# Kernel optimization log

Hardware: AMD Instinct MI355X
Metric: run time of the kernel (lower is better)

## Reference

```python
import jax, jax.numpy as jnp
import numpy as np

DIM = 2048
DIM_SEQ = 2048
DIM_OUT = DIM // 2
LN_EPS = 1e-5


def setup_inputs() -> dict:
    key = jax.random.key(0)
    k1, k2 = jax.random.split(key)
    x = jax.random.normal(k1, (8, DIM_SEQ, DIM), dtype=jnp.float32)
    init_eps = 0.001 / DIM_SEQ
    # Conv1d(dim_seq, dim_seq, 1) weight -> [seq, seq] seq-mixing matrix
    proj_w = jax.random.uniform(k2, (DIM_SEQ, DIM_SEQ), minval=-init_eps, maxval=init_eps, dtype=jnp.float32)
    proj_b = jnp.ones((DIM_SEQ,), dtype=jnp.float32)
    ln_scale = jnp.ones((DIM_OUT,), dtype=jnp.float32)
    ln_bias = jnp.zeros((DIM_OUT,), dtype=jnp.float32)
    return {"x": x, "proj_w": proj_w, "proj_b": proj_b, "ln_scale": ln_scale, "ln_bias": ln_bias}


def reference(x, proj_w, proj_b, ln_scale, ln_bias):
    # chunk into residual and gate halves along feature dim
    res, gate = jnp.split(x, 2, axis=-1)  # each [b, s, d/2]
    # LayerNorm over last dim of gate
    mu = jnp.mean(gate, axis=-1, keepdims=True)
    var = jnp.mean(jnp.square(gate - mu), axis=-1, keepdims=True)
    gate = (gate - mu) * jax.lax.rsqrt(var + LN_EPS) * ln_scale + ln_bias
    # Conv1d kernel=1 over seq axis == seq-mixing matmul: [s,t] x [b,t,d] -> [b,s,d]
    gate = jnp.einsum('st,btd->bsd', proj_w, gate) + proj_b[None, :, None]
    # act = Identity; gated residual multiply
    return gate * res
```

## Files before the change

### kernel.cpp

```cpp
#include <hip/hip_runtime.h>

typedef __attribute__((ext_vector_type(4))) float floatx4;
typedef __attribute__((ext_vector_type(2))) unsigned long ulongx2;

__device__ __forceinline__ unsigned short f2bf(float f) {
    unsigned int u = __builtin_bit_cast(unsigned int, f);
    u += 0x7fffu + ((u >> 16) & 1u);
    return (unsigned short)(u >> 16);
}

__device__ __forceinline__ float bf2f(unsigned short u) {
    return __builtin_bit_cast(float, ((unsigned int)u) << 16);
}

__device__ __forceinline__ void async16(void* lds, const void* g) {
    __builtin_amdgcn_global_load_lds(
        (const __attribute__((address_space(1))) void*)(g),
        (__attribute__((address_space(3))) void*)(lds),
        16, 0, 0);
}

#define DIM      2048
#define DSEQ     2048
#define DOUT     1024
#define NBATCH   8
#define NKT      (DSEQ / 64)
#define WSCALE   4194304.0f
#define WINV     (1.0f / 4194304.0f)


__global__ __launch_bounds__(256) void cast_w_kernel(const float* __restrict__ w,
                                                     unsigned char* __restrict__ o) {
    int i = (blockIdx.x * 256 + threadIdx.x) * 4;
    int s = i >> 11;
    int t = i & 2047;
    float4 v = *(const float4*)(w + i);
    int w0 = __builtin_amdgcn_cvt_pk_fp8_f32(v.x * WSCALE, v.y * WSCALE, 0, false);
    w0     = __builtin_amdgcn_cvt_pk_fp8_f32(v.z * WSCALE, v.w * WSCALE, w0, true);
    unsigned char* dst = o + (((size_t)(t >> 6)) * DSEQ + s) * 64
                           + ((t >> 3) & 3) * 16 + ((t >> 5) & 1) * 8 + (t & 7);
    *(unsigned int*)dst = (unsigned int)w0;
}

__global__ __launch_bounds__(256) void ln_t_kernel(const float* __restrict__ X,
                                                   const float* __restrict__ lns,
                                                   const float* __restrict__ lnb,
                                                   unsigned char* __restrict__ Gt) {
    const int tid  = threadIdx.x;
    const int wave = tid >> 6;
    const int lane = tid & 63;
    const int t0   = blockIdx.x * 32;
    const int b    = blockIdx.y;
    const int kt   = t0 >> 6;
    const int h    = (t0 >> 5) & 1;

    __shared__ unsigned short lt[32][1028];

    float4 sc[4], bi[4];
    #pragma unroll
    for (int c = 0; c < 4; ++c) {
        sc[c] = *(const float4*)(lns + c * 256 + lane * 4);
        bi[c] = *(const float4*)(lnb + c * 256 + lane * 4);
    }

    #pragma unroll 1
    for (int i = 0; i < 8; ++i) {
        const int r = wave * 8 + i;
        const float* xr = X + ((size_t)(b * DSEQ + t0 + r)) * DIM + DOUT;
        float4 v[4];
        float s = 0.f, ss = 0.f;
        #pragma unroll
        for (int c = 0; c < 4; ++c) {
            v[c] = *(const float4*)(xr + c * 256 + lane * 4);
            s  += v[c].x + v[c].y + v[c].z + v[c].w;
            ss += v[c].x * v[c].x + v[c].y * v[c].y + v[c].z * v[c].z + v[c].w * v[c].w;
        }
        #pragma unroll
        for (int off = 32; off > 0; off >>= 1) {
            s  += __shfl_xor(s,  off, 64);
            ss += __shfl_xor(ss, off, 64);
        }
        const float mu  = s * (1.f / 1024.f);
        const float var = ss * (1.f / 1024.f) - mu * mu;
        const float inv = rsqrtf(var + 1e-5f);
        #pragma unroll
        for (int c = 0; c < 4; ++c) {
            const int d = c * 256 + lane * 4;
            float y0 = (v[c].x - mu) * inv * sc[c].x + bi[c].x;
            float y1 = (v[c].y - mu) * inv * sc[c].y + bi[c].y;
            float y2 = (v[c].z - mu) * inv * sc[c].z + bi[c].z;
            float y3 = (v[c].w - mu) * inv * sc[c].w + bi[c].w;
            unsigned int lo = (unsigned int)f2bf(y0) | ((unsigned int)f2bf(y1) << 16);
            unsigned int hi = (unsigned int)f2bf(y2) | ((unsigned int)f2bf(y3) << 16);
            *(uint2*)&lt[r][d] = make_uint2(lo, hi);
        }
    }
    __syncthreads();

    #pragma unroll
    for (int it = 0; it < 4; ++it) {
        const int d = it * 256 + tid;
        unsigned char* dst = Gt + (((size_t)b * NKT + kt) * DOUT + d) * 64 + h * 8;
        #pragma unroll
        for (int qq = 0; qq < 4; ++qq) {
            const int lr = qq * 8;
            int w0 = __builtin_amdgcn_cvt_pk_fp8_f32(bf2f(lt[lr + 0][d]), bf2f(lt[lr + 1][d]), 0, false);
            w0     = __builtin_amdgcn_cvt_pk_fp8_f32(bf2f(lt[lr + 2][d]), bf2f(lt[lr + 3][d]), w0, true);
            int w1 = __builtin_amdgcn_cvt_pk_fp8_f32(bf2f(lt[lr + 4][d]), bf2f(lt[lr + 5][d]), 0, false);
            w1     = __builtin_amdgcn_cvt_pk_fp8_f32(bf2f(lt[lr + 6][d]), bf2f(lt[lr + 7][d]), w1, true);
            *(uint2*)(dst + qq * 16) = make_uint2((unsigned int)w0, (unsigned int)w1);
        }
    }
}

#define BM 128
#define BN 128

__global__ __launch_bounds__(256, 3) void gemm_sgu(const unsigned char* __restrict__ Wt,
                                                   const unsigned char* __restrict__ Gt,
                                                   const float* __restrict__ X,
                                                   const float* __restrict__ Pb,
                                                   float* __restrict__ Out) {
    const int tid = threadIdx.x;
    const int ys  = blockIdx.x & 7;
    const int xs  = (blockIdx.x >> 3) | (blockIdx.y << 1);
    const int s0  = xs * BM;
    const int d0  = ys * BN;
    const int b   = blockIdx.z;

    __shared__ __align__(16) unsigned char smem[32768];

    const int wave = tid >> 6;
    const int lane = tid & 63;
    const int wr   = wave >> 1;
    const int wc   = wave & 1;
    const int ln15 = lane & 15;
    const int q    = lane >> 4;

    int ldsOff[2], srcA[2], srcB[2];
    #pragma unroll
    for (int j = 0; j < 2; ++j) {
        const int c  = tid + j * 256;
        const int r  = c >> 2;
        const int kc = (c & 3) ^ (r & 3);
        ldsOff[j] = c * 16;
        srcA[j]   = (s0 + r) * 64 + kc * 16;
        srcB[j]   = (d0 + r) * 64 + kc * 16;
    }
    int aOff[4], bOff[4];
    #pragma unroll
    for (int i = 0; i < 4; ++i) {
        const int ra = wr * 64 + i * 16 + ln15;
        const int rb = wc * 64 + i * 16 + ln15;
        aOff[i] = ra * 64 + ((q ^ (ra & 3)) * 16);
        bOff[i] = rb * 64 + ((q ^ (rb & 3)) * 16);
    }

    floatx4 acc[4][4] = {};

    const unsigned char* gB = Gt + (size_t)b * (NKT * DOUT * 64);

    {
        unsigned char* As = smem;
        unsigned char* Bs = smem + 8192;
        #pragma unroll
        for (int j = 0; j < 2; ++j) {
            async16(As + ldsOff[j], Wt + srcA[j]);
            async16(Bs + ldsOff[j], gB + srcB[j]);
        }
    }

    for (int t = 0; t < NKT; ++t) {
        unsigned char* Ab = smem + (t & 1) * 16384;
        unsigned char* Bb = Ab + 8192;
        __syncthreads();

        if (t + 1 < NKT) {
            const unsigned char* aB0 = Wt + (size_t)(t + 1) * (DSEQ * 64);
            const unsigned char* bB0 = gB + (size_t)(t + 1) * (DOUT * 64);
            unsigned char* An = smem + ((t + 1) & 1) * 16384;
            unsigned char* Bn = An + 8192;
            #pragma unroll
            for (int j = 0; j < 2; ++j) {
                async16(An + ldsOff[j], aB0 + srcA[j]);
                async16(Bn + ldsOff[j], bB0 + srcB[j]);
            }
        }

        ulongx2 a2[4], b2[4];
        #pragma unroll
        for (int i = 0; i < 4; ++i) a2[i] = *(const ulongx2*)(Ab + aOff[i]);
        #pragma unroll
        for (int i = 0; i < 4; ++i) b2[i] = *(const ulongx2*)(Bb + bOff[i]);
        #pragma unroll
        for (int i = 0; i < 4; ++i)
            #pragma unroll
            for (int j = 0; j < 4; ++j)
                acc[i][j] = __builtin_amdgcn_mfma_f32_16x16x32_fp8_fp8(
                    (long)a2[i].x, (long)b2[j].x, acc[i][j], 0, 0, 0);
        #pragma unroll
        for (int i = 0; i < 4; ++i)
            #pragma unroll
            for (int j = 0; j < 4; ++j)
                acc[i][j] = __builtin_amdgcn_mfma_f32_16x16x32_fp8_fp8(
                    (long)a2[i].y, (long)b2[j].y, acc[i][j], 0, 0, 0);
    }

    float (*ep)[132] = (float (*)[132])smem;
    const int gr  = tid >> 3;
    const int seg = tid & 7;
    #pragma unroll
    for (int e = 0; e < 4; ++e) {
        __syncthreads();
        #pragma unroll
        for (int j = 0; j < 4; ++j) {
            const int C = wc * 64 + j * 16 + ln15;
            #pragma unroll
            for (int r = 0; r < 4; ++r)
                ep[wr * 16 + q * 4 + r][C] = acc[e][j][r];
        }
        __syncthreads();
        const int s = s0 + (gr >> 4) * 64 + e * 16 + (gr & 15);
        const int d = d0 + seg * 16;
        const float pb = Pb[s];
        const float* xr = X + ((size_t)(b * DSEQ + s)) * DIM + d;
        float*       orow = Out + ((size_t)(b * DSEQ + s)) * DOUT + d;
        #pragma unroll
        for (int w = 0; w < 4; ++w) {
            float4 c = *(const float4*)&ep[gr][seg * 16 + w * 4];
            float4 x = *(const float4*)(xr + w * 4);
            float4 o;
            o.x = (c.x * WINV + pb) * x.x;
            o.y = (c.y * WINV + pb) * x.y;
            o.z = (c.z * WINV + pb) * x.z;
            o.w = (c.w * WINV + pb) * x.w;
            *(float4*)(orow + w * 4) = o;
        }
    }
}

extern "C" void kernel_launch(void* const* d_in, const int* in_sizes, int n_in,
                              void* d_out, int out_size, void* d_ws, size_t ws_size,
                              hipStream_t stream) {
    const float* x    = (const float*)d_in[0];
    const float* pw   = (const float*)d_in[1];
    const float* pb   = (const float*)d_in[2];
    const float* lns  = (const float*)d_in[3];
    const float* lnb  = (const float*)d_in[4];
    float* out        = (float*)d_out;

    unsigned char* Wt = (unsigned char*)d_ws;
    unsigned char* Gt = (unsigned char*)d_ws + (size_t)DSEQ * DSEQ;

    cast_w_kernel<<<dim3((DSEQ * DSEQ) / 1024), dim3(256), 0, stream>>>(pw, Wt);
    ln_t_kernel<<<dim3(DSEQ / 32, NBATCH), dim3(256), 0, stream>>>(x, lns, lnb, Gt);
    gemm_sgu<<<dim3(16, 8, NBATCH), dim3(256), 0, stream>>>(Wt, Gt, x, pb, out);
}
```

Measured before the change: 271.9 us.

## Switch GEMM to gfx950 scaled 16x16x128 FP8 MFMA with K=128 tiles

```diff
diff --git a/kernel.cpp b/kernel.cpp
--- a/kernel.cpp
+++ b/kernel.cpp
@@ -1,7 +1,8 @@
 #include <hip/hip_runtime.h>
 
 typedef __attribute__((ext_vector_type(4))) float floatx4;
-typedef __attribute__((ext_vector_type(2))) unsigned long ulongx2;
+typedef __attribute__((ext_vector_type(4))) int   intx4;
+typedef __attribute__((ext_vector_type(8))) int   intx8;
 
 __device__ __forceinline__ unsigned short f2bf(float f) {
     unsigned int u = __builtin_bit_cast(unsigned int, f);
@@ -24,9 +25,10 @@
 #define DSEQ     2048
 #define DOUT     1024
 #define NBATCH   8
-#define NKT      (DSEQ / 64)
+#define NKT      (DSEQ / 128)
 #define WSCALE   4194304.0f
 #define WINV     (1.0f / 4194304.0f)
+#define UNIT_SCALE 0x7F7F7F7F
 
 
 __global__ __launch_bounds__(256) void cast_w_kernel(const float* __restrict__ w,
@@ -37,8 +39,7 @@
     float4 v = *(const float4*)(w + i);
     int w0 = __builtin_amdgcn_cvt_pk_fp8_f32(v.x * WSCALE, v.y * WSCALE, 0, false);
     w0     = __builtin_amdgcn_cvt_pk_fp8_f32(v.z * WSCALE, v.w * WSCALE, w0, true);
-    unsigned char* dst = o + (((size_t)(t >> 6)) * DSEQ + s) * 64
-                           + ((t >> 3) & 3) * 16 + ((t >> 5) & 1) * 8 + (t & 7);
+    unsigned char* dst = o + (((size_t)(t >> 7)) * DSEQ + s) * 128 + (t & 127);
     *(unsigned int*)dst = (unsigned int)w0;
 }
 
@@ -51,8 +52,8 @@
     const int lane = tid & 63;
     const int t0   = blockIdx.x * 32;
     const int b    = blockIdx.y;
-    const int kt   = t0 >> 6;
-    const int h    = (t0 >> 5) & 1;
+    const int kt   = t0 >> 7;
+    const int h2   = (t0 >> 5) & 3;
 
     __shared__ unsigned short lt[32][1028];
 
@@ -100,23 +101,24 @@
     #pragma unroll
     for (int it = 0; it < 4; ++it) {
         const int d = it * 256 + tid;
-        unsigned char* dst = Gt + (((size_t)b * NKT + kt) * DOUT + d) * 64 + h * 8;
-        #pragma unroll
-        for (int qq = 0; qq < 4; ++qq) {
-            const int lr = qq * 8;
+        unsigned int u[8];
+        #pragma unroll
+        for (int g = 0; g < 8; ++g) {
+            const int lr = g * 4;
             int w0 = __builtin_amdgcn_cvt_pk_fp8_f32(bf2f(lt[lr + 0][d]), bf2f(lt[lr + 1][d]), 0, false);
             w0     = __builtin_amdgcn_cvt_pk_fp8_f32(bf2f(lt[lr + 2][d]), bf2f(lt[lr + 3][d]), w0, true);
-            int w1 = __builtin_amdgcn_cvt_pk_fp8_f32(bf2f(lt[lr + 4][d]), bf2f(lt[lr + 5][d]), 0, false);
-            w1     = __builtin_amdgcn_cvt_pk_fp8_f32(bf2f(lt[lr + 6][d]), bf2f(lt[lr + 7][d]), w1, true);
-            *(uint2*)(dst + qq * 16) = make_uint2((unsigned int)w0, (unsigned int)w1);
-        }
+            u[g] = (unsigned int)w0;
+        }
+        unsigned char* dst = Gt + (((size_t)b * NKT + kt) * DOUT + d) * 128 + h2 * 32;
+        *(uint4*)(dst)      = make_uint4(u[0], u[1], u[2], u[3]);
+        *(uint4*)(dst + 16) = make_uint4(u[4], u[5], u[6], u[7]);
     }
 }
 
 #define BM 128
 #define BN 128
 
-__global__ __launch_bounds__(256, 3) void gemm_sgu(const unsigned char* __restrict__ Wt,
+__global__ __launch_bounds__(256, 2) void gemm_sgu(const unsigned char* __restrict__ Wt,
                                                    const unsigned char* __restrict__ Gt,
                                                    const float* __restrict__ X,
                                                    const float* __restrict__ Pb,
@@ -128,7 +130,7 @@
     const int d0  = ys * BN;
     const int b   = blockIdx.z;
 
-    __shared__ __align__(16) unsigned char smem[32768];
+    __shared__ __align__(16) unsigned char smem[65536];
 
     const int wave = tid >> 6;
     const int lane = tid & 63;
@@ -137,73 +139,79 @@
     const int ln15 = lane & 15;
     const int q    = lane >> 4;
 
-    int ldsOff[2], srcA[2], srcB[2];
-    #pragma unroll
-    for (int j = 0; j < 2; ++j) {
+    int ldsOff[4], srcA[4], srcB[4];
+    #pragma unroll
+    for (int j = 0; j < 4; ++j) {
         const int c  = tid + j * 256;
-        const int r  = c >> 2;
-        const int kc = (c & 3) ^ (r & 3);
+        const int r  = c >> 3;
+        const int kc = (c & 7) ^ (r & 7);
         ldsOff[j] = c * 16;
-        srcA[j]   = (s0 + r) * 64 + kc * 16;
-        srcB[j]   = (d0 + r) * 64 + kc * 16;
-    }
-    int aOff[4], bOff[4];
+        srcA[j]   = (s0 + r) * 128 + kc * 16;
+        srcB[j]   = (d0 + r) * 128 + kc * 16;
+    }
+    int aOff0[4], aOff1[4], bOff0[4], bOff1[4];
     #pragma unroll
     for (int i = 0; i < 4; ++i) {
         const int ra = wr * 64 + i * 16 + ln15;
         const int rb = wc * 64 + i * 16 + ln15;
-        aOff[i] = ra * 64 + ((q ^ (ra & 3)) * 16);
-        bOff[i] = rb * 64 + ((q ^ (rb & 3)) * 16);
+        aOff0[i] = ra * 128 + ((2 * q)     ^ (ra & 7)) * 16;
+        aOff1[i] = ra * 128 + ((2 * q + 1) ^ (ra & 7)) * 16;
+        bOff0[i] = rb * 128 + ((2 * q)     ^ (rb & 7)) * 16;
+        bOff1[i] = rb * 128 + ((2 * q + 1) ^ (rb & 7)) * 16;
     }
 
     floatx4 acc[4][4] = {};
 
-    const unsigned char* gB = Gt + (size_t)b * (NKT * DOUT * 64);
+    const unsigned char* gB = Gt + (size_t)b * ((size_t)NKT * DOUT * 128);
 
     {
         unsigned char* As = smem;
-        unsigned char* Bs = smem + 8192;
-        #pragma unroll
-        for (int j = 0; j < 2; ++j) {
+        unsigned char* Bs = smem + 16384;
+        #pragma unroll
+        for (int j = 0; j < 4; ++j) {
             async16(As + ldsOff[j], Wt + srcA[j]);
             async16(Bs + ldsOff[j], gB + srcB[j]);
         }
     }
 
     for (int t = 0; t < NKT; ++t) {
-        unsigned char* Ab = smem + (t & 1) * 16384;
-        unsigned char* Bb = Ab + 8192;
+        unsigned char* Ab = smem + (t & 1) * 32768;
+        unsigned char* Bb = Ab + 16384;
         __syncthreads();
 
         if (t + 1 < NKT) {
-            const unsigned char* aB0 = Wt + (size_t)(t + 1) * (DSEQ * 64);
-            const unsigned char* bB0 = gB + (size_t)(t + 1) * (DOUT * 64);
-            unsigned char* An = smem + ((t + 1) & 1) * 16384;
-            unsigned char* Bn = An + 8192;
+            const unsigned char* aB0 = Wt + (size_t)(t + 1) * (DSEQ * 128);
+            const unsigned char* bB0 = gB + (size_t)(t + 1) * (DOUT * 128);
+            unsigned char* An = smem + ((t + 1) & 1) * 32768;
+            unsigned char* Bn = An + 16384;
             #pragma unroll
-            for (int j = 0; j < 2; ++j) {
+            for (int j = 0; j < 4; ++j) {
                 async16(An + ldsOff[j], aB0 + srcA[j]);
                 async16(Bn + ldsOff[j], bB0 + srcB[j]);
             }
         }
 
-        ulongx2 a2[4], b2[4];
-        #pragma unroll
-        for (int i = 0; i < 4; ++i) a2[i] = *(const ulongx2*)(Ab + aOff[i]);
-        #pragma unroll
-        for (int i = 0; i < 4; ++i) b2[i] = *(const ulongx2*)(Bb + bOff[i]);
+        intx8 a8[4], b8[4];
+        #pragma unroll
+        for (int i = 0; i < 4; ++i) {
+            intx4 lo = *(const intx4*)(Ab + aOff0[i]);
+            intx4 hi = *(const intx4*)(Ab + aOff1[i]);
+            a8[i] = __builtin_shufflevector(lo, hi, 0, 1, 2, 3, 4, 5, 6, 7);
+        }
+        #pragma unroll
+        for (int i = 0; i < 4; ++i) {
+            intx4 lo = *(const intx4*)(Bb + bOff0[i]);
+            intx4 hi = *(const intx4*)(Bb + bOff1[i]);
+            b8[i] = __builtin_shufflevector(lo, hi, 0, 1, 2, 3, 4, 5, 6, 7);
+        }
         #pragma unroll
         for (int i = 0; i < 4; ++i)
             #pragma unroll
             for (int j = 0; j < 4; ++j)
-                acc[i][j] = __builtin_amdgcn_mfma_f32_16x16x32_fp8_fp8(
-                    (long)a2[i].x, (long)b2[j].x, acc[i][j], 0, 0, 0);
-        #pragma unroll
-        for (int i = 0; i < 4; ++i)
-            #pragma unroll
-            for (int j = 0; j < 4; ++j)
-                acc[i][j] = __builtin_amdgcn_mfma_f32_16x16x32_fp8_fp8(
-                    (long)a2[i].y, (long)b2[j].y, acc[i][j], 0, 0, 0);
+                acc[i][j] = __builtin_amdgcn_mfma_scale_f32_16x16x128_f8f6f4(
+                    a8[i], b8[j], acc[i][j],
+                    0 , 0 ,
+                    0, UNIT_SCALE, 0, UNIT_SCALE);
     }
 
     float (*ep)[132] = (float (*)[132])smem;
```

After: 264.1 us. -2.9%, faster.
